# Kernel tuning notes

Measured on AMD Instinct MI355X. Metric: run time of the kernel, lower is better.

## Reference

```python
import jax, jax.numpy as jnp
import numpy as np

N_NODES = 100000
N_EDGES = 1600000
IN_C = 256
H1 = 128
H2 = 64
OUT_C = 64


def setup_inputs() -> dict:
    key = jax.random.key(0)
    ks = jax.random.split(key, 8)
    x = jax.random.normal(ks[0], (N_NODES, IN_C), dtype=jnp.float32)
    edge_src = jax.random.randint(ks[1], (N_EDGES,), 0, N_NODES, dtype=jnp.int32)
    edge_dst = jax.random.randint(ks[2], (N_EDGES,), 0, N_NODES, dtype=jnp.int32)
    edge_weight = jax.random.uniform(ks[3], (N_EDGES,), dtype=jnp.float32)
    W1 = jax.random.normal(ks[4], (IN_C, H1), dtype=jnp.float32) / np.sqrt(IN_C)
    b1 = jnp.zeros((H1,), dtype=jnp.float32)
    W2 = jax.random.normal(ks[5], (H1, H2), dtype=jnp.float32) / np.sqrt(H1)
    b2 = jnp.zeros((H2,), dtype=jnp.float32)
    W3 = jax.random.normal(ks[6], (H2, OUT_C), dtype=jnp.float32) / np.sqrt(H2)
    b3 = jnp.zeros((OUT_C,), dtype=jnp.float32)
    return dict(x=x, edge_src=edge_src, edge_dst=edge_dst, edge_weight=edge_weight,
                W1=W1, b1=b1, W2=W2, b2=b2, W3=W3, b3=b3)


def _gcn_layer(h, W, b, src, dst, ew):
    # GraphConvolution: out = adj @ (h @ W) + b, adj given as weighted edge list
    support = h @ W                      # [N, d_out] dense GEMM
    msg = support[src] * ew[:, None]     # [E, d_out] gather (irregular access)
    agg = jax.ops.segment_sum(msg, dst, num_segments=N_NODES)  # SpMM scatter-add
    return agg + b


def reference(x, edge_src, edge_dst, edge_weight, W1, b1, W2, b2, W3, b3):
    # Eval-mode forward: dropout is identity (training=False)
    h = jax.nn.relu(_gcn_layer(x, W1, b1, edge_src, edge_dst, edge_weight))
    h = jax.nn.relu(_gcn_layer(h, W2, b2, edge_src, edge_dst, edge_weight))
    out = _gcn_layer(h, W3, b3, edge_src, edge_dst, edge_weight)
    return out
```

## Files before the change

kernel.cpp:

```cpp
#include <hip/hip_runtime.h>
#include <hip/hip_bf16.h>


#define EPB 8192

typedef unsigned int u32x2 __attribute__((ext_vector_type(2)));

__device__ __forceinline__ unsigned short f2bf(float f) {
    unsigned int u = __float_as_uint(f);
    unsigned int r = (u + 0x7fffu + ((u >> 16) & 1u)) >> 16;
    return (unsigned short)r;
}

using frag_ab = __attribute__((ext_vector_type(8))) short;
using frag_cd = __attribute__((ext_vector_type(4))) float;

__global__ __launch_bounds__(256) void prep_kernel(
    const float* __restrict__ W1, const float* __restrict__ W2, const float* __restrict__ W3,
    unsigned short* __restrict__ WT1, unsigned short* __restrict__ WT2, unsigned short* __restrict__ WT3,
    const float* __restrict__ x, unsigned short* __restrict__ Xb, int total8)
{
    const int b = blockIdx.x;
    if (b < 176) {
        const int i = b * 256 + threadIdx.x;
        const float* W; unsigned short* WT; int K, N, j;
        if (i < 32768)      { W = W1; WT = WT1; K = 256; N = 128; j = i; }
        else if (i < 40960) { W = W2; WT = WT2; K = 128; N = 64;  j = i - 32768; }
        else                { W = W3; WT = WT3; K = 64;  N = 64;  j = i - 40960; }
        const int n = j / K, k = j % K;
        WT[j] = f2bf(W[k * N + n]);
    } else {
        const int i = (b - 176) * 256 + threadIdx.x;
        if (i >= total8) return;
        const float4 a = *(const float4*)&x[(size_t)i * 8];
        const float4 c = *(const float4*)&x[(size_t)i * 8 + 4];
        uint4 u;
        u.x = ((unsigned)f2bf(a.y) << 16) | (unsigned)f2bf(a.x);
        u.y = ((unsigned)f2bf(a.w) << 16) | (unsigned)f2bf(a.z);
        u.z = ((unsigned)f2bf(c.y) << 16) | (unsigned)f2bf(c.x);
        u.w = ((unsigned)f2bf(c.w) << 16) | (unsigned)f2bf(c.z);
        *(uint4*)&Xb[(size_t)i * 8] = u;
    }
}

template <int BN, int K, int WAVES>
__global__ __launch_bounds__(WAVES * 64) void wgemm_kernel(
    const unsigned short* __restrict__ A, const unsigned short* __restrict__ WT,
    unsigned short* __restrict__ C, int M)
{
    constexpr int LDB = K + 8;
    constexpr int NKS = K / 32;
    constexpr int KB = (NKS >= 8) ? 8 : NKS;
    constexpr int NB = NKS / KB;
    __shared__ unsigned short Bs[BN * LDB];

    const int tid = threadIdx.x;
    const int wave = tid >> 6;
    const int lane = tid & 63;
    const int quad = lane >> 4;
    const int l16 = lane & 15;

    constexpr int NTHR = WAVES * 64;
    constexpr int TOT = BN * K / 8;
    for (int i = tid; i < TOT; i += NTHR) {
        const int n = (i << 3) / K;
        const int c = (i << 3) & (K - 1);
        *(uint4*)&Bs[n * LDB + c] = *(const uint4*)&WT[(size_t)n * K + c];
    }
    __syncthreads();

    const int tiles = (M + 15) >> 4;
    for (int tile = blockIdx.x * WAVES + wave; tile < tiles; tile += gridDim.x * WAVES) {
        const int r0 = tile * 16 + l16;
        const bool rv = r0 < M;
        const unsigned short* base = &A[(size_t)r0 * K + quad * 8];

        frag_cd acc[BN / 16];
#pragma unroll
        for (int f = 0; f < BN / 16; ++f) acc[f] = (frag_cd){0.f, 0.f, 0.f, 0.f};

#pragma unroll
        for (int b = 0; b < NB; ++b) {
            frag_ab af[KB];
#pragma unroll
            for (int k = 0; k < KB; ++k) {
                const int ks = b * KB + k;
                frag_ab f8 = (frag_ab){0, 0, 0, 0, 0, 0, 0, 0};
                if (rv) f8 = *(const frag_ab*)(base + ks * 32);
                af[k] = f8;
            }
#pragma unroll
            for (int k = 0; k < KB; ++k) {
                const int kk = (b * KB + k) * 32 + quad * 8;
#pragma unroll
                for (int f = 0; f < BN / 16; ++f) {
                    const frag_ab bf = *(const frag_ab*)&Bs[(f * 16 + l16) * LDB + kk];
                    acc[f] = __builtin_amdgcn_mfma_f32_16x16x32_bf16(af[k], bf, acc[f], 0, 0, 0);
                }
            }
        }

#pragma unroll
        for (int f = 0; f < BN / 16; ++f)
#pragma unroll
            for (int r = 0; r < 4; ++r) {
                const int row = tile * 16 + quad * 4 + r;
                if (row < M) C[(size_t)row * BN + f * 16 + l16] = f2bf(acc[f][r]);
            }
    }
}

__global__ __launch_bounds__(256) void count_kernel(
    const int* __restrict__ dst, int* __restrict__ cmat, int E, int nblk, int nbuck)
{
    __shared__ int hist[1600];
    for (int i = threadIdx.x; i < nbuck; i += 256) hist[i] = 0;
    __syncthreads();
    const int base = blockIdx.x * EPB;
    const int end = min(base + EPB, E);
    for (int e = base + threadIdx.x; e < end; e += 256)
        atomicAdd(&hist[dst[e] >> 6], 1);
    __syncthreads();
    for (int i = threadIdx.x; i < nbuck; i += 256)
        cmat[(size_t)i * nblk + blockIdx.x] = hist[i];
}

__global__ __launch_bounds__(256) void scanA_kernel(
    int* __restrict__ data, int* __restrict__ psum, int L)
{
    __shared__ int tmp[256];
    const int b0 = blockIdx.x * 1024 + threadIdx.x * 4;
    int v[4] = {0, 0, 0, 0};
    if (b0 + 3 < L) { const int4 t = *(const int4*)&data[b0]; v[0]=t.x; v[1]=t.y; v[2]=t.z; v[3]=t.w; }
    else { for (int i = 0; i < 4; ++i) if (b0 + i < L) v[i] = data[b0 + i]; }
    const int s = v[0] + v[1] + v[2] + v[3];
    tmp[threadIdx.x] = s;
    __syncthreads();
#pragma unroll
    for (int d = 1; d < 256; d <<= 1) {
        const int t = (threadIdx.x >= d) ? tmp[threadIdx.x - d] : 0;
        __syncthreads();
        tmp[threadIdx.x] += t;
        __syncthreads();
    }
    int run = tmp[threadIdx.x] - s;
    int o[4];
#pragma unroll
    for (int i = 0; i < 4; ++i) { o[i] = run; run += v[i]; }
    if (b0 + 3 < L) { *(int4*)&data[b0] = make_int4(o[0], o[1], o[2], o[3]); }
    else { for (int i = 0; i < 4; ++i) if (b0 + i < L) data[b0 + i] = o[i]; }
    if (threadIdx.x == 255) psum[blockIdx.x] = tmp[255];
}

__global__ __launch_bounds__(1024) void scanB_kernel(int* __restrict__ psum, int nb)
{
    __shared__ int tmp[1024];
    const int v = ((int)threadIdx.x < nb) ? psum[threadIdx.x] : 0;
    tmp[threadIdx.x] = v;
    __syncthreads();
#pragma unroll
    for (int d = 1; d < 1024; d <<= 1) {
        const int t = ((int)threadIdx.x >= d) ? tmp[threadIdx.x - d] : 0;
        __syncthreads();
        tmp[threadIdx.x] += t;
        __syncthreads();
    }
    if ((int)threadIdx.x < nb) psum[threadIdx.x] = tmp[threadIdx.x] - v;
}

__global__ __launch_bounds__(256) void scanC_kernel(
    int* __restrict__ data, const int* __restrict__ psum, int L)
{
    const int i = blockIdx.x * 256 + threadIdx.x;
    if (i < L) data[i] += psum[i >> 10];
}

__global__ __launch_bounds__(256) void place_kernel(
    const int* __restrict__ src, const int* __restrict__ dst, const float* __restrict__ ew,
    const int* __restrict__ cmat, uint2* __restrict__ ebuck, int E, int nblk, int nbuck)
{
    __shared__ int cursor[1600];
    const int k = blockIdx.x;
    for (int i = threadIdx.x; i < nbuck; i += 256)
        cursor[i] = cmat[(size_t)i * nblk + k];
    __syncthreads();
    const int base = k * EPB;
    const int end = min(base + EPB, E);
    for (int e = base + threadIdx.x; e < end; e += 256) {
        const int d = dst[e];
        const int b = d >> 6;
        const int pos = atomicAdd(&cursor[b], 1);
        ebuck[pos] = make_uint2(((unsigned)src[e] << 6) | (unsigned)(d & 63),
                                __float_as_uint(ew[e]));
    }
}

__global__ __launch_bounds__(256) void sort2_kernel(
    const uint2* __restrict__ ebuck, const int* __restrict__ cmat,
    int* __restrict__ offs, uint2* __restrict__ ecsr,
    int N, int nblk, int nbuck, int E)
{
    __shared__ int cnt[64];
    __shared__ int cur[64];
    const int b = blockIdx.x;
    const int node0 = b << 6;
    const int nn = min(64, N - node0);
    const int j0 = cmat[(size_t)b * nblk];
    const int j1 = (b + 1 < nbuck) ? cmat[(size_t)(b + 1) * nblk] : E;

    if (threadIdx.x < 64) cnt[threadIdx.x] = 0;
    __syncthreads();
    for (int j = j0 + (int)threadIdx.x; j < j1; j += 256)
        atomicAdd(&cnt[ebuck[j].x & 63u], 1);
    __syncthreads();

    if (threadIdx.x < 64) {
        const int myv = cnt[threadIdx.x];
        int v = myv;
#pragma unroll
        for (int d = 1; d < 64; d <<= 1) {
            const int t = __shfl_up(v, d, 64);
            if ((int)threadIdx.x >= d) v += t;
        }
        const int base = j0 + v - myv;
        cur[threadIdx.x] = base;
        if ((int)threadIdx.x < nn) offs[node0 + threadIdx.x] = base;
        if (threadIdx.x == 0 && b == nbuck - 1) offs[N] = E;
    }
    __syncthreads();

    for (int j = j0 + (int)threadIdx.x; j < j1; j += 256) {
        const uint2 ed = ebuck[j];
        const int pos = atomicAdd(&cur[ed.x & 63u], 1);
        ecsr[pos] = make_uint2(ed.x >> 6, ed.y);
    }
}

template <int D, int LOGT, bool RELU, typename OUT_T>
__global__ __launch_bounds__(256) void gather_agg_kernel(
    const unsigned short* __restrict__ S, const int* __restrict__ offs,
    const uint2* __restrict__ ecsr,
    const float* __restrict__ bias, OUT_T* __restrict__ out, int N)
{
    constexpr int TPN = 1 << LOGT;
    constexpr int NPRE = 32 / TPN;
    const int gid = blockIdx.x * 256 + threadIdx.x;
    const int node = gid >> LOGT;
    if (node >= N) return;
    const int lane = gid & (TPN - 1);
    const int c8 = lane << 3;

    const int j0 = offs[node];
    const int j1 = offs[node + 1];

    float acc[8];
#pragma unroll
    for (int c = 0; c < 8; ++c) acc[c] = 0.f;

    if (j0 < j1) {
        const int jlast = j1 - 1;

        int   mc[NPRE];
        float mw[NPRE];
#pragma unroll
        for (int ch = 0; ch < NPRE; ++ch) {
            const int j = j0 + ch * TPN + lane;
            const u32x2 p = *(const u32x2*)&ecsr[min(j, jlast)];
            mc[ch] = (int)p.x;
            mw[ch] = (j <= jlast) ? __uint_as_float(p.y) : 0.f;
        }
#pragma unroll
        for (int ch = 0; ch < NPRE; ++ch) {
            if (j0 + ch * TPN < j1) {
#pragma unroll
                for (int t = 0; t < TPN; ++t) {
                    const int s = __shfl(mc[ch], t, TPN);
                    const float w = __shfl(mw[ch], t, TPN);
                    const uint4 v = *(const uint4*)&S[(size_t)s * D + c8];
#pragma unroll
                    for (int q = 0; q < 4; ++q) {
                        const unsigned int u = (&v.x)[q];
                        acc[q * 2 + 0] += w * __uint_as_float(u << 16);
                        acc[q * 2 + 1] += w * __uint_as_float(u & 0xffff0000u);
                    }
                }
            }
        }
        for (int jb = j0 + NPRE * TPN; jb < j1; jb += TPN) {
            const int j = jb + lane;
            const u32x2 p = *(const u32x2*)&ecsr[min(j, jlast)];
            const int myc = (int)p.x;
            const float myw = (j <= jlast) ? __uint_as_float(p.y) : 0.f;
#pragma unroll
            for (int t = 0; t < TPN; ++t) {
                const int s = __shfl(myc, t, TPN);
                const float w = __shfl(myw, t, TPN);
                const uint4 v = *(const uint4*)&S[(size_t)s * D + c8];
#pragma unroll
                for (int q = 0; q < 4; ++q) {
                    const unsigned int u = (&v.x)[q];
                    acc[q * 2 + 0] += w * __uint_as_float(u << 16);
                    acc[q * 2 + 1] += w * __uint_as_float(u & 0xffff0000u);
                }
            }
        }
    }

#pragma unroll
    for (int c = 0; c < 8; ++c) {
        float v = acc[c] + bias[c8 + c];
        if (RELU) v = fmaxf(v, 0.f);
        acc[c] = v;
    }
    if constexpr (sizeof(OUT_T) == 2) {
        uint4 u;
        u.x = ((unsigned)f2bf(acc[1]) << 16) | (unsigned)f2bf(acc[0]);
        u.y = ((unsigned)f2bf(acc[3]) << 16) | (unsigned)f2bf(acc[2]);
        u.z = ((unsigned)f2bf(acc[5]) << 16) | (unsigned)f2bf(acc[4]);
        u.w = ((unsigned)f2bf(acc[7]) << 16) | (unsigned)f2bf(acc[6]);
        *(uint4*)&((unsigned short*)out)[(size_t)node * D + c8] = u;
    } else {
        float* op = (float*)out + (size_t)node * D + c8;
        *(float4*)op = make_float4(acc[0], acc[1], acc[2], acc[3]);
        *((float4*)op + 1) = make_float4(acc[4], acc[5], acc[6], acc[7]);
    }
}

extern "C" void kernel_launch(void* const* d_in, const int* in_sizes, int n_in,
                              void* d_out, int out_size, void* d_ws, size_t ws_size,
                              hipStream_t stream)
{
    const float* x    = (const float*)d_in[0];
    const int*   esrc = (const int*)  d_in[1];
    const int*   edst = (const int*)  d_in[2];
    const float* ew   = (const float*)d_in[3];
    const float* W1   = (const float*)d_in[4];
    const float* b1   = (const float*)d_in[5];
    const float* W2   = (const float*)d_in[6];
    const float* b2   = (const float*)d_in[7];
    const float* W3   = (const float*)d_in[8];
    const float* b3   = (const float*)d_in[9];

    const int N = in_sizes[0] / 256;
    const int E = in_sizes[1];

    const int nbuck = (N + 63) >> 6;
    const int nblk = (E + EPB - 1) / EPB;
    const int L = nbuck * nblk;

    unsigned short* Xb = (unsigned short*)d_ws;
    unsigned short* Hb = Xb;
    unsigned short* Sb = Xb + (size_t)N * 256;
    unsigned short* WT1 = Sb + (size_t)N * 128;
    unsigned short* WT2 = WT1 + 256 * 128;
    unsigned short* WT3 = WT2 + 128 * 64;
    uint2* ebuck = (uint2*)(WT3 + 64 * 64);
    uint2* ecsr  = ebuck + E;
    int* offs   = (int*)(ecsr + E);
    int* cmat   = offs + N + 4;
    int* psum   = cmat + ((L + 3) & ~3);
    float* out  = (float*)d_out;

    const dim3 blk(256);
    const int tiles = (N + 15) >> 4;
    const int total8 = N * 256 / 8;

    prep_kernel<<<176 + (total8 + 255) / 256, blk, 0, stream>>>(
        W1, W2, W3, WT1, WT2, WT3, x, Xb, total8);
    count_kernel<<<nblk, blk, 0, stream>>>(edst, cmat, E, nblk, nbuck);
    scanA_kernel<<<(L + 1023) / 1024, blk, 0, stream>>>(cmat, psum, L);
    scanB_kernel<<<1, 1024, 0, stream>>>(psum, (L + 1023) / 1024);
    scanC_kernel<<<(L + 255) / 256, blk, 0, stream>>>(cmat, psum, L);
    place_kernel<<<nblk, blk, 0, stream>>>(esrc, edst, ew, cmat, ebuck, E, nblk, nbuck);
    sort2_kernel<<<nbuck, blk, 0, stream>>>(ebuck, cmat, offs, ecsr, N, nblk, nbuck, E);

    wgemm_kernel<128, 256, 8><<<512, dim3(512), 0, stream>>>(Xb, WT1, Sb, N);
    gather_agg_kernel<128, 4, true, unsigned short><<<((N * 16) + 255) / 256, blk, 0, stream>>>(
        Sb, offs, ecsr, b1, Hb, N);

    wgemm_kernel<64, 128, 4><<<(tiles + 3) / 4, blk, 0, stream>>>(Hb, WT2, Sb, N);
    gather_agg_kernel<64, 3, true, unsigned short><<<((N * 8) + 255) / 256, blk, 0, stream>>>(
        Sb, offs, ecsr, b2, Hb, N);

    wgemm_kernel<64, 64, 4><<<(tiles + 3) / 4, blk, 0, stream>>>(Hb, WT3, Sb, N);
    gather_agg_kernel<64, 3, false, float><<<((N * 8) + 255) / 256, blk, 0, stream>>>(
        Sb, offs, ecsr, b3, out, N);
}
```

Baseline: 466.6 us.

## Fold scan add-back into consumers and halve per-thread width in gather

Drops the scanC kernel by having place_kernel and sort2_kernel add the block prefix from psum themselves when they read cmat. The gather/aggregate kernels now give each thread 4 channels (8-byte loads) instead of 8, doubling the threads per node and with them parallelism and memory-level concurrency. NPRE becomes 32/TPN, so it shrinks, and the prefetch depth per thread changes. Each edge index and weight is also shuffled across twice as many lanes.

```diff
diff --git a/kernel.cpp b/kernel.cpp
--- a/kernel.cpp
+++ b/kernel.cpp
@@ -168,21 +168,17 @@
     if ((int)threadIdx.x < nb) psum[threadIdx.x] = tmp[threadIdx.x] - v;
 }
 
-__global__ __launch_bounds__(256) void scanC_kernel(
-    int* __restrict__ data, const int* __restrict__ psum, int L)
-{
-    const int i = blockIdx.x * 256 + threadIdx.x;
-    if (i < L) data[i] += psum[i >> 10];
-}
-
 __global__ __launch_bounds__(256) void place_kernel(
     const int* __restrict__ src, const int* __restrict__ dst, const float* __restrict__ ew,
-    const int* __restrict__ cmat, uint2* __restrict__ ebuck, int E, int nblk, int nbuck)
+    const int* __restrict__ cmat, const int* __restrict__ psum,
+    uint2* __restrict__ ebuck, int E, int nblk, int nbuck)
 {
     __shared__ int cursor[1600];
     const int k = blockIdx.x;
-    for (int i = threadIdx.x; i < nbuck; i += 256)
-        cursor[i] = cmat[(size_t)i * nblk + k];
+    for (int i = threadIdx.x; i < nbuck; i += 256) {
+        const size_t idx = (size_t)i * nblk + k;
+        cursor[i] = cmat[idx] + psum[idx >> 10];
+    }
     __syncthreads();
     const int base = k * EPB;
     const int end = min(base + EPB, E);
@@ -196,7 +192,7 @@
 }
 
 __global__ __launch_bounds__(256) void sort2_kernel(
-    const uint2* __restrict__ ebuck, const int* __restrict__ cmat,
+    const uint2* __restrict__ ebuck, const int* __restrict__ cmat, const int* __restrict__ psum,
     int* __restrict__ offs, uint2* __restrict__ ecsr,
     int N, int nblk, int nbuck, int E)
 {
@@ -205,8 +201,13 @@
     const int b = blockIdx.x;
     const int node0 = b << 6;
     const int nn = min(64, N - node0);
-    const int j0 = cmat[(size_t)b * nblk];
-    const int j1 = (b + 1 < nbuck) ? cmat[(size_t)(b + 1) * nblk] : E;
+    const size_t i0 = (size_t)b * nblk;
+    const int j0 = cmat[i0] + psum[i0 >> 10];
+    int j1 = E;
+    if (b + 1 < nbuck) {
+        const size_t i1 = (size_t)(b + 1) * nblk;
+        j1 = cmat[i1] + psum[i1 >> 10];
+    }
 
     if (threadIdx.x < 64) cnt[threadIdx.x] = 0;
     __syncthreads();
@@ -248,14 +249,12 @@
     const int node = gid >> LOGT;
     if (node >= N) return;
     const int lane = gid & (TPN - 1);
-    const int c8 = lane << 3;
+    const int c4 = lane << 2;
 
     const int j0 = offs[node];
     const int j1 = offs[node + 1];
 
-    float acc[8];
-#pragma unroll
-    for (int c = 0; c < 8; ++c) acc[c] = 0.f;
+    float acc[4] = {0.f, 0.f, 0.f, 0.f};
 
     if (j0 < j1) {
         const int jlast = j1 - 1;
@@ -276,13 +275,11 @@
                 for (int t = 0; t < TPN; ++t) {
                     const int s = __shfl(mc[ch], t, TPN);
                     const float w = __shfl(mw[ch], t, TPN);
-                    const uint4 v = *(const uint4*)&S[(size_t)s * D + c8];
-#pragma unroll
-                    for (int q = 0; q < 4; ++q) {
-                        const unsigned int u = (&v.x)[q];
-                        acc[q * 2 + 0] += w * __uint_as_float(u << 16);
-                        acc[q * 2 + 1] += w * __uint_as_float(u & 0xffff0000u);
-                    }
+                    const u32x2 v = *(const u32x2*)&S[(size_t)s * D + c4];
+                    acc[0] += w * __uint_as_float(v.x << 16);
+                    acc[1] += w * __uint_as_float(v.x & 0xffff0000u);
+                    acc[2] += w * __uint_as_float(v.y << 16);
+                    acc[3] += w * __uint_as_float(v.y & 0xffff0000u);
                 }
             }
         }
@@ -295,34 +292,29 @@
             for (int t = 0; t < TPN; ++t) {
                 const int s = __shfl(myc, t, TPN);
                 const float w = __shfl(myw, t, TPN);
-                const uint4 v = *(const uint4*)&S[(size_t)s * D + c8];
-#pragma unroll
-                for (int q = 0; q < 4; ++q) {
-                    const unsigned int u = (&v.x)[q];
-                    acc[q * 2 + 0] += w * __uint_as_float(u << 16);
-                    acc[q * 2 + 1] += w * __uint_as_float(u & 0xffff0000u);
-                }
-            }
-        }
-    }
-
-#pragma unroll
-    for (int c = 0; c < 8; ++c) {
-        float v = acc[c] + bias[c8 + c];
+                const u32x2 v = *(const u32x2*)&S[(size_t)s * D + c4];
+                acc[0] += w * __uint_as_float(v.x << 16);
+                acc[1] += w * __uint_as_float(v.x & 0xffff0000u);
+                acc[2] += w * __uint_as_float(v.y << 16);
+                acc[3] += w * __uint_as_float(v.y & 0xffff0000u);
+            }
+        }
+    }
+
+#pragma unroll
+    for (int c = 0; c < 4; ++c) {
+        float v = acc[c] + bias[c4 + c];
         if (RELU) v = fmaxf(v, 0.f);
         acc[c] = v;
     }
     if constexpr (sizeof(OUT_T) == 2) {
-        uint4 u;
+        u32x2 u;
         u.x = ((unsigned)f2bf(acc[1]) << 16) | (unsigned)f2bf(acc[0]);
         u.y = ((unsigned)f2bf(acc[3]) << 16) | (unsigned)f2bf(acc[2]);
-        u.z = ((unsigned)f2bf(acc[5]) << 16) | (unsigned)f2bf(acc[4]);
-        u.w = ((unsigned)f2bf(acc[7]) << 16) | (unsigned)f2bf(acc[6]);
-        *(uint4*)&((unsigned short*)out)[(size_t)node * D + c8] = u;
+        *(u32x2*)&((unsigned short*)out)[(size_t)node * D + c4] = u;
     } else {
-        float* op = (float*)out + (size_t)node * D + c8;
+        float* op = (float*)out + (size_t)node * D + c4;
         *(float4*)op = make_float4(acc[0], acc[1], acc[2], acc[3]);
-        *((float4*)op + 1) = make_float4(acc[4], acc[5], acc[6], acc[7]);
     }
 }
 
@@ -370,19 +362,18 @@
     count_kernel<<<nblk, blk, 0, stream>>>(edst, cmat, E, nblk, nbuck);
     scanA_kernel<<<(L + 1023) / 1024, blk, 0, stream>>>(cmat, psum, L);
     scanB_kernel<<<1, 1024, 0, stream>>>(psum, (L + 1023) / 1024);
-    scanC_kernel<<<(L + 255) / 256, blk, 0, stream>>>(cmat, psum, L);
-    place_kernel<<<nblk, blk, 0, stream>>>(esrc, edst, ew, cmat, ebuck, E, nblk, nbuck);
-    sort2_kernel<<<nbuck, blk, 0, stream>>>(ebuck, cmat, offs, ecsr, N, nblk, nbuck, E);
+    place_kernel<<<nblk, blk, 0, stream>>>(esrc, edst, ew, cmat, psum, ebuck, E, nblk, nbuck);
+    sort2_kernel<<<nbuck, blk, 0, stream>>>(ebuck, cmat, psum, offs, ecsr, N, nblk, nbuck, E);
 
     wgemm_kernel<128, 256, 8><<<512, dim3(512), 0, stream>>>(Xb, WT1, Sb, N);
-    gather_agg_kernel<128, 4, true, unsigned short><<<((N * 16) + 255) / 256, blk, 0, stream>>>(
+    gather_agg_kernel<128, 5, true, unsigned short><<<((N * 32) + 255) / 256, blk, 0, stream>>>(
         Sb, offs, ecsr, b1, Hb, N);
 
     wgemm_kernel<64, 128, 4><<<(tiles + 3) / 4, blk, 0, stream>>>(Hb, WT2, Sb, N);
-    gather_agg_kernel<64, 3, true, unsigned short><<<((N * 8) + 255) / 256, blk, 0, stream>>>(
+    gather_agg_kernel<64, 4, true, unsigned short><<<((N * 16) + 255) / 256, blk, 0, stream>>>(
         Sb, offs, ecsr, b2, Hb, N);
 
     wgemm_kernel<64, 64, 4><<<(tiles + 3) / 4, blk, 0, stream>>>(Hb, WT3, Sb, N);
-    gather_agg_kernel<64, 3, false, float><<<((N * 8) + 255) / 256, blk, 0, stream>>>(
+    gather_agg_kernel<64, 4, false, float><<<((N * 16) + 255) / 256, blk, 0, stream>>>(
         Sb, offs, ecsr, b3, out, N);
 }
```

Measured after the change: 472.9 us. No clear change (+1.3%).
